# Optimization experiments

Measured on AMD Instinct MI355X. Metric: run time of the kernel, lower is better.

The kernel has to match this reference:

```python
import jax, jax.numpy as jnp
import numpy as np

VEC_DIM = 300
NUM_DOCS = 500000
NUM_WORDS = 100000
BATCH = 4096
NUM_CTX = 10
NUM_NOISE_P1 = 26


def setup_inputs() -> dict:
    key = jax.random.key(0)
    k1, k2, k3, k4, k5 = jax.random.split(key, 5)
    context_ids = jax.random.randint(k1, (BATCH, NUM_CTX), 0, NUM_WORDS)
    doc_ids = jax.random.randint(k2, (BATCH,), 0, NUM_DOCS)
    target_noise_ids = jax.random.randint(k3, (BATCH, NUM_NOISE_P1), 0, NUM_WORDS)
    D = jax.random.normal(k4, (NUM_DOCS, VEC_DIM), dtype=jnp.float32)
    W = jax.random.normal(k5, (NUM_WORDS, VEC_DIM), dtype=jnp.float32)
    O = jnp.zeros((VEC_DIM, NUM_WORDS), dtype=jnp.float32)
    return {
        "context_ids": context_ids,
        "doc_ids": doc_ids,
        "target_noise_ids": target_noise_ids,
        "D": D,
        "W": W,
        "O": O,
    }


def reference(context_ids, doc_ids, target_noise_ids, D, W, O):
    # x[b] = D[doc_ids[b]] + sum_c W[context_ids[b, c]]   -> (B, vec_dim)
    x = D[doc_ids] + jnp.sum(W[context_ids], axis=1)
    # O[:, target_noise_ids] gathered as O.T[target_noise_ids] -> (B, N, vec_dim)
    # scores[b, n] = x[b] . O[:, target_noise_ids[b, n]]
    scores = jnp.einsum("bd,bnd->bn", x, O.T[target_noise_ids])
    return scores
```

## Files before the change

kernel.cpp:

```cpp
#include <hip/hip_runtime.h>

#define VEC_DIM   300
#define VEC_F4    75
#define NUM_WORDS 100000
#define BATCH_N   4096
#define NUM_CTX   10
#define NUM_NOISE 26
#define TWORDS    32

__global__ __launch_bounds__(256) void transpose_kernel(
    const float* __restrict__ O,
    float*       __restrict__ OT)
{
    __shared__ float tile[TWORDS * VEC_DIM];
    const int wBase = blockIdx.x * TWORDS;
    const int tid   = threadIdx.x;

    for (int idx = tid; idx < VEC_DIM * (TWORDS / 4); idx += 256) {
        const int d = idx >> 3;
        const int c = idx & 7;
        const float4 v = *reinterpret_cast<const float4*>(
            O + (size_t)d * NUM_WORDS + wBase + 4 * c);
        tile[(4 * c + 0) * VEC_DIM + d] = v.x;
        tile[(4 * c + 1) * VEC_DIM + d] = v.y;
        tile[(4 * c + 2) * VEC_DIM + d] = v.z;
        tile[(4 * c + 3) * VEC_DIM + d] = v.w;
    }
    __syncthreads();

    for (int idx = tid; idx < TWORDS * VEC_F4; idx += 256) {
        const int w = idx / VEC_F4;
        const int c = idx - w * VEC_F4;
        const float4 v = *reinterpret_cast<const float4*>(tile + w * VEC_DIM + 4 * c);
        *reinterpret_cast<float4*>(OT + (size_t)(wBase + w) * VEC_DIM + 4 * c) = v;
    }
}

__global__ __launch_bounds__(256) void pvdm_score_kernel(
    const int*   __restrict__ context_ids,
    const int*   __restrict__ doc_ids,
    const int*   __restrict__ tn_ids,
    const float* __restrict__ D,
    const float* __restrict__ W,
    const float* __restrict__ OT,
    float*       __restrict__ out)
{
    __shared__ float4 xs4[VEC_F4];
    const int b   = blockIdx.x;
    const int tid = threadIdx.x;

    if (tid < VEC_F4) {
        const int doc = doc_ids[b];
        const float4* __restrict__ Drow =
            reinterpret_cast<const float4*>(D + (size_t)doc * VEC_DIM);
        float4 v = Drow[tid];
#pragma unroll
        for (int c = 0; c < NUM_CTX; ++c) {
            const int wd = context_ids[b * NUM_CTX + c];
            const float4 u =
                reinterpret_cast<const float4*>(W + (size_t)wd * VEC_DIM)[tid];
            v.x += u.x; v.y += u.y; v.z += u.z; v.w += u.w;
        }
        xs4[tid] = v;
    }
    __syncthreads();

    const int wave = tid >> 6;
    const int lane = tid & 63;

    const float4 xa = xs4[lane];
    float4 xb = make_float4(0.f, 0.f, 0.f, 0.f);
    if (lane < VEC_F4 - 64) xb = xs4[64 + lane];

    const int* __restrict__ tb = tn_ids + b * NUM_NOISE;

#pragma unroll
    for (int k = 0; k < 7; ++k) {
        const int n = wave + 4 * k;
        if (n < NUM_NOISE) {
            const int t = tb[n];
            const float4* __restrict__ row =
                reinterpret_cast<const float4*>(OT + (size_t)t * VEC_DIM);
            const float4 ra = row[lane];
            float s = ra.x * xa.x + ra.y * xa.y + ra.z * xa.z + ra.w * xa.w;
            if (lane < VEC_F4 - 64) {
                const float4 rb = row[64 + lane];
                s += rb.x * xb.x + rb.y * xb.y + rb.z * xb.z + rb.w * xb.w;
            }
#pragma unroll
            for (int off = 32; off > 0; off >>= 1)
                s += __shfl_down(s, off, 64);
            if (lane == 0) out[b * NUM_NOISE + n] = s;
        }
    }
}

__global__ __launch_bounds__(256) void pvdm_score_direct_kernel(
    const int*   __restrict__ context_ids,
    const int*   __restrict__ doc_ids,
    const int*   __restrict__ tn_ids,
    const float* __restrict__ D,
    const float* __restrict__ W,
    const float* __restrict__ O,
    float*       __restrict__ out)
{
    __shared__ float xs[VEC_DIM];
    const int b   = blockIdx.x;
    const int tid = threadIdx.x;
    const int doc = doc_ids[b];
    int ctx[NUM_CTX];
#pragma unroll
    for (int c = 0; c < NUM_CTX; ++c) ctx[c] = context_ids[b * NUM_CTX + c];
    for (int d = tid; d < VEC_DIM; d += 256) {
        float v = D[(size_t)doc * VEC_DIM + d];
#pragma unroll
        for (int c = 0; c < NUM_CTX; ++c)
            v += W[(size_t)ctx[c] * VEC_DIM + d];
        xs[d] = v;
    }
    __syncthreads();
    const int wave = tid >> 6;
    const int lane = tid & 63;
    for (int n = wave; n < NUM_NOISE; n += 4) {
        const int t = tn_ids[b * NUM_NOISE + n];
        float s = 0.0f;
        for (int d = lane; d < VEC_DIM; d += 64)
            s += xs[d] * O[(size_t)d * NUM_WORDS + t];
#pragma unroll
        for (int off = 32; off > 0; off >>= 1)
            s += __shfl_down(s, off, 64);
        if (lane == 0) out[b * NUM_NOISE + n] = s;
    }
}

extern "C" void kernel_launch(void* const* d_in, const int* in_sizes, int n_in,
                              void* d_out, int out_size, void* d_ws, size_t ws_size,
                              hipStream_t stream) {
    const int*   context_ids = (const int*)  d_in[0];
    const int*   doc_ids     = (const int*)  d_in[1];
    const int*   tn_ids      = (const int*)  d_in[2];
    const float* D           = (const float*)d_in[3];
    const float* W           = (const float*)d_in[4];
    const float* O           = (const float*)d_in[5];
    float*       out         = (float*)d_out;

    const size_t OT_BYTES = (size_t)NUM_WORDS * VEC_DIM * sizeof(float);

    if (ws_size >= OT_BYTES) {
        float* OT = (float*)d_ws;
        transpose_kernel<<<NUM_WORDS / TWORDS, 256, 0, stream>>>(O, OT);
        pvdm_score_kernel<<<BATCH_N, 256, 0, stream>>>(
            context_ids, doc_ids, tn_ids, D, W, OT, out);
    } else {
        pvdm_score_direct_kernel<<<BATCH_N, 256, 0, stream>>>(
            context_ids, doc_ids, tn_ids, D, W, O, out);
    }
}
```

Measured before the change: 809.2 us.

## Drop O transpose pass and gather strided columns of O directly

```diff
diff --git a/kernel.cpp b/kernel.cpp
--- a/kernel.cpp
+++ b/kernel.cpp
@@ -7,6 +7,72 @@
 #define NUM_CTX   10
 #define NUM_NOISE 26
 #define TWORDS    32
+
+
+__global__ __launch_bounds__(256) void pvdm_score_direct_kernel(
+    const int*   __restrict__ context_ids,
+    const int*   __restrict__ doc_ids,
+    const int*   __restrict__ tn_ids,
+    const float* __restrict__ D,
+    const float* __restrict__ W,
+    const float* __restrict__ O,
+    float*       __restrict__ out)
+{
+    __shared__ __align__(16) float xs[VEC_DIM];
+    const int b   = blockIdx.x;
+    const int tid = threadIdx.x;
+
+    if (tid < VEC_F4) {
+        const int doc = doc_ids[b];
+        float4 v = reinterpret_cast<const float4*>(D + (size_t)doc * VEC_DIM)[tid];
+#pragma unroll
+        for (int c = 0; c < NUM_CTX; ++c) {
+            const int wd = context_ids[b * NUM_CTX + c];
+            const float4 u =
+                reinterpret_cast<const float4*>(W + (size_t)wd * VEC_DIM)[tid];
+            v.x += u.x; v.y += u.y; v.z += u.z; v.w += u.w;
+        }
+        reinterpret_cast<float4*>(xs)[tid] = v;
+    }
+    __syncthreads();
+
+    const int wave = tid >> 6;
+    const int lane = tid & 63;
+
+    const float x0 = xs[lane];
+    const float x1 = xs[lane + 64];
+    const float x2 = xs[lane + 128];
+    const float x3 = xs[lane + 192];
+    const float x4 = (lane < VEC_DIM - 256) ? xs[lane + 256] : 0.0f;
+
+    const int* __restrict__ tb = tn_ids + b * NUM_NOISE;
+
+    int tv[7];
+#pragma unroll
+    for (int k = 0; k < 7; ++k) {
+        const int n = wave + 4 * k;
+        tv[k] = (n < NUM_NOISE) ? tb[n] : tb[0];
+    }
+
+#pragma unroll
+    for (int k = 0; k < 7; ++k) {
+        const int n = wave + 4 * k;
+        if (n < NUM_NOISE) {
+            const float* __restrict__ col = O + tv[k];
+            float s = x0 * col[(size_t)(lane      ) * NUM_WORDS]
+                    + x1 * col[(size_t)(lane +  64) * NUM_WORDS]
+                    + x2 * col[(size_t)(lane + 128) * NUM_WORDS]
+                    + x3 * col[(size_t)(lane + 192) * NUM_WORDS];
+            if (lane < VEC_DIM - 256)
+                s += x4 * col[(size_t)(lane + 256) * NUM_WORDS];
+#pragma unroll
+            for (int off = 32; off > 0; off >>= 1)
+                s += __shfl_down(s, off, 64);
+            if (lane == 0) out[b * NUM_NOISE + n] = s;
+        }
+    }
+}
+
 
 __global__ __launch_bounds__(256) void transpose_kernel(
     const float* __restrict__ O,
@@ -51,9 +117,7 @@
 
     if (tid < VEC_F4) {
         const int doc = doc_ids[b];
-        const float4* __restrict__ Drow =
-            reinterpret_cast<const float4*>(D + (size_t)doc * VEC_DIM);
-        float4 v = Drow[tid];
+        float4 v = reinterpret_cast<const float4*>(D + (size_t)doc * VEC_DIM)[tid];
 #pragma unroll
         for (int c = 0; c < NUM_CTX; ++c) {
             const int wd = context_ids[b * NUM_CTX + c];
@@ -95,44 +159,6 @@
     }
 }
 
-__global__ __launch_bounds__(256) void pvdm_score_direct_kernel(
-    const int*   __restrict__ context_ids,
-    const int*   __restrict__ doc_ids,
-    const int*   __restrict__ tn_ids,
-    const float* __restrict__ D,
-    const float* __restrict__ W,
-    const float* __restrict__ O,
-    float*       __restrict__ out)
-{
-    __shared__ float xs[VEC_DIM];
-    const int b   = blockIdx.x;
-    const int tid = threadIdx.x;
-    const int doc = doc_ids[b];
-    int ctx[NUM_CTX];
-#pragma unroll
-    for (int c = 0; c < NUM_CTX; ++c) ctx[c] = context_ids[b * NUM_CTX + c];
-    for (int d = tid; d < VEC_DIM; d += 256) {
-        float v = D[(size_t)doc * VEC_DIM + d];
-#pragma unroll
-        for (int c = 0; c < NUM_CTX; ++c)
-            v += W[(size_t)ctx[c] * VEC_DIM + d];
-        xs[d] = v;
-    }
-    __syncthreads();
-    const int wave = tid >> 6;
-    const int lane = tid & 63;
-    for (int n = wave; n < NUM_NOISE; n += 4) {
-        const int t = tn_ids[b * NUM_NOISE + n];
-        float s = 0.0f;
-        for (int d = lane; d < VEC_DIM; d += 64)
-            s += xs[d] * O[(size_t)d * NUM_WORDS + t];
-#pragma unroll
-        for (int off = 32; off > 0; off >>= 1)
-            s += __shfl_down(s, off, 64);
-        if (lane == 0) out[b * NUM_NOISE + n] = s;
-    }
-}
-
 extern "C" void kernel_launch(void* const* d_in, const int* in_sizes, int n_in,
                               void* d_out, int out_size, void* d_ws, size_t ws_size,
                               hipStream_t stream) {
@@ -144,15 +170,7 @@
     const float* O           = (const float*)d_in[5];
     float*       out         = (float*)d_out;
 
-    const size_t OT_BYTES = (size_t)NUM_WORDS * VEC_DIM * sizeof(float);
-
-    if (ws_size >= OT_BYTES) {
-        float* OT = (float*)d_ws;
-        transpose_kernel<<<NUM_WORDS / TWORDS, 256, 0, stream>>>(O, OT);
-        pvdm_score_kernel<<<BATCH_N, 256, 0, stream>>>(
-            context_ids, doc_ids, tn_ids, D, W, OT, out);
-    } else {
-        pvdm_score_direct_kernel<<<BATCH_N, 256, 0, stream>>>(
-            context_ids, doc_ids, tn_ids, D, W, O, out);
-    }
+    (void)d_ws; (void)ws_size;
+    pvdm_score_direct_kernel<<<BATCH_N, 256, 0, stream>>>(
+        context_ids, doc_ids, tn_ids, D, W, O, out);
 }
```

After: 1.289 ms. 1.59x slower.

## Bucket noise targets by word chunk and score against one streamed pass of O

Applied to the files above, without the earlier changes.

```diff
diff --git a/kernel.cpp b/kernel.cpp
--- a/kernel.cpp
+++ b/kernel.cpp
@@ -2,20 +2,124 @@
 
 #define VEC_DIM   300
 #define VEC_F4    75
+#define NUM_DOCS  500000
 #define NUM_WORDS 100000
 #define BATCH_N   4096
 #define NUM_CTX   10
 #define NUM_NOISE 26
-#define TWORDS    32
+
+#define WB        32
+#define NCHUNK    (NUM_WORDS / WB)
+#define CAP       192
+
+#define WS_X_OFF        0
+#define WS_CNT_OFF      (8u << 20)
+#define WS_BKT_OFF      ((8u << 20) + (64u << 10))
+#define WS_NEEDED       (WS_BKT_OFF + (size_t)NCHUNK * CAP * 4)
+
+__global__ __launch_bounds__(256) void zero_counters_kernel(int* __restrict__ cnt)
+{
+    const int i = blockIdx.x * 256 + threadIdx.x;
+    if (i < NCHUNK) cnt[i] = 0;
+}
+
+__global__ __launch_bounds__(128) void build_scatter_kernel(
+    const int*   __restrict__ context_ids,
+    const int*   __restrict__ doc_ids,
+    const int*   __restrict__ tn_ids,
+    const float* __restrict__ D,
+    const float* __restrict__ W,
+    float*       __restrict__ X,
+    int*         __restrict__ counters,
+    unsigned*    __restrict__ buckets)
+{
+    const int b   = blockIdx.x;
+    const int tid = threadIdx.x;
+
+    if (tid < VEC_F4) {
+        const int doc = doc_ids[b];
+        float4 v = reinterpret_cast<const float4*>(D + (size_t)doc * VEC_DIM)[tid];
+#pragma unroll
+        for (int c = 0; c < NUM_CTX; ++c) {
+            const int wd = context_ids[b * NUM_CTX + c];
+            const float4 u =
+                reinterpret_cast<const float4*>(W + (size_t)wd * VEC_DIM)[tid];
+            v.x += u.x; v.y += u.y; v.z += u.z; v.w += u.w;
+        }
+        reinterpret_cast<float4*>(X + (size_t)b * VEC_DIM)[tid] = v;
+    } else if (tid < VEC_F4 + NUM_NOISE) {
+        const int n = tid - VEC_F4;
+        const int t = tn_ids[b * NUM_NOISE + n];
+        const int chunk = t >> 5;
+        const int tc    = t & (WB - 1);
+        const int pos   = atomicAdd(&counters[chunk], 1);
+        if (pos < CAP)
+            buckets[(size_t)chunk * CAP + pos] =
+                ((unsigned)b << 10) | ((unsigned)n << 5) | (unsigned)tc;
+    }
+}
+
+__global__ __launch_bounds__(256) void chunk_score_kernel(
+    const float*    __restrict__ O,
+    const float*    __restrict__ X,
+    const int*      __restrict__ counters,
+    const unsigned* __restrict__ buckets,
+    float*          __restrict__ out)
+{
+    __shared__ float tile[WB][VEC_DIM];
+    const int chunk = blockIdx.x;
+    const int tid   = threadIdx.x;
+    const int w0    = chunk * WB;
+
+    int cnt = counters[chunk];
+    if (cnt > CAP) cnt = CAP;
+
+#pragma unroll
+    for (int k = 0; k < 10; ++k) {
+        const int d  = (tid >> 3) + (k << 5);
+        const int jj = tid & 7;
+        if (d < VEC_DIM) {
+            const float4 v = *reinterpret_cast<const float4*>(
+                O + (size_t)d * NUM_WORDS + w0 + 4 * jj);
+            tile[4 * jj + 0][d] = v.x;
+            tile[4 * jj + 1][d] = v.y;
+            tile[4 * jj + 2][d] = v.z;
+            tile[4 * jj + 3][d] = v.w;
+        }
+    }
+    __syncthreads();
+
+    const int wave = tid >> 6;
+    const int lane = tid & 63;
+
+    for (int p = wave; p < cnt; p += 4) {
+        const unsigned e = buckets[(size_t)chunk * CAP + p];
+        const int tc = e & 31;
+        const int n  = (e >> 5) & 31;
+        const int b  = e >> 10;
+        const float* __restrict__ xr = X + (size_t)b * VEC_DIM;
+
+        float s = tile[tc][lane]       * xr[lane]
+                + tile[tc][lane +  64] * xr[lane +  64]
+                + tile[tc][lane + 128] * xr[lane + 128]
+                + tile[tc][lane + 192] * xr[lane + 192];
+        if (lane < VEC_DIM - 256)
+            s += tile[tc][lane + 256] * xr[lane + 256];
+#pragma unroll
+        for (int off = 32; off > 0; off >>= 1)
+            s += __shfl_down(s, off, 64);
+        if (lane == 0) out[b * NUM_NOISE + n] = s;
+    }
+}
+
+#define TWORDS 32
 
 __global__ __launch_bounds__(256) void transpose_kernel(
-    const float* __restrict__ O,
-    float*       __restrict__ OT)
+    const float* __restrict__ O, float* __restrict__ OT)
 {
     __shared__ float tile[TWORDS * VEC_DIM];
     const int wBase = blockIdx.x * TWORDS;
     const int tid   = threadIdx.x;
-
     for (int idx = tid; idx < VEC_DIM * (TWORDS / 4); idx += 256) {
         const int d = idx >> 3;
         const int c = idx & 7;
@@ -27,7 +131,6 @@
         tile[(4 * c + 3) * VEC_DIM + d] = v.w;
     }
     __syncthreads();
-
     for (int idx = tid; idx < TWORDS * VEC_F4; idx += 256) {
         const int w = idx / VEC_F4;
         const int c = idx - w * VEC_F4;
@@ -37,23 +140,17 @@
 }
 
 __global__ __launch_bounds__(256) void pvdm_score_kernel(
-    const int*   __restrict__ context_ids,
-    const int*   __restrict__ doc_ids,
-    const int*   __restrict__ tn_ids,
-    const float* __restrict__ D,
-    const float* __restrict__ W,
-    const float* __restrict__ OT,
-    float*       __restrict__ out)
+    const int* __restrict__ context_ids, const int* __restrict__ doc_ids,
+    const int* __restrict__ tn_ids, const float* __restrict__ D,
+    const float* __restrict__ W, const float* __restrict__ OT,
+    float* __restrict__ out)
 {
     __shared__ float4 xs4[VEC_F4];
     const int b   = blockIdx.x;
     const int tid = threadIdx.x;
-
     if (tid < VEC_F4) {
         const int doc = doc_ids[b];
-        const float4* __restrict__ Drow =
-            reinterpret_cast<const float4*>(D + (size_t)doc * VEC_DIM);
-        float4 v = Drow[tid];
+        float4 v = reinterpret_cast<const float4*>(D + (size_t)doc * VEC_DIM)[tid];
 #pragma unroll
         for (int c = 0; c < NUM_CTX; ++c) {
             const int wd = context_ids[b * NUM_CTX + c];
@@ -64,16 +161,12 @@
         xs4[tid] = v;
     }
     __syncthreads();
-
     const int wave = tid >> 6;
     const int lane = tid & 63;
-
     const float4 xa = xs4[lane];
     float4 xb = make_float4(0.f, 0.f, 0.f, 0.f);
     if (lane < VEC_F4 - 64) xb = xs4[64 + lane];
-
     const int* __restrict__ tb = tn_ids + b * NUM_NOISE;
-
 #pragma unroll
     for (int k = 0; k < 7; ++k) {
         const int n = wave + 4 * k;
@@ -96,13 +189,10 @@
 }
 
 __global__ __launch_bounds__(256) void pvdm_score_direct_kernel(
-    const int*   __restrict__ context_ids,
-    const int*   __restrict__ doc_ids,
-    const int*   __restrict__ tn_ids,
-    const float* __restrict__ D,
-    const float* __restrict__ W,
-    const float* __restrict__ O,
-    float*       __restrict__ out)
+    const int* __restrict__ context_ids, const int* __restrict__ doc_ids,
+    const int* __restrict__ tn_ids, const float* __restrict__ D,
+    const float* __restrict__ W, const float* __restrict__ O,
+    float* __restrict__ out)
 {
     __shared__ float xs[VEC_DIM];
     const int b   = blockIdx.x;
@@ -144,9 +234,18 @@
     const float* O           = (const float*)d_in[5];
     float*       out         = (float*)d_out;
 
-    const size_t OT_BYTES = (size_t)NUM_WORDS * VEC_DIM * sizeof(float);
-
-    if (ws_size >= OT_BYTES) {
+    if (ws_size >= WS_NEEDED) {
+        char* ws = (char*)d_ws;
+        float*    X        = (float*)   (ws + WS_X_OFF);
+        int*      counters = (int*)     (ws + WS_CNT_OFF);
+        unsigned* buckets  = (unsigned*)(ws + WS_BKT_OFF);
+
+        zero_counters_kernel<<<(NCHUNK + 255) / 256, 256, 0, stream>>>(counters);
+        build_scatter_kernel<<<BATCH_N, 128, 0, stream>>>(
+            context_ids, doc_ids, tn_ids, D, W, X, counters, buckets);
+        chunk_score_kernel<<<NCHUNK, 256, 0, stream>>>(
+            O, X, counters, buckets, out);
+    } else if (ws_size >= (size_t)NUM_WORDS * VEC_DIM * sizeof(float)) {
         float* OT = (float*)d_ws;
         transpose_kernel<<<NUM_WORDS / TWORDS, 256, 0, stream>>>(O, OT);
         pvdm_score_kernel<<<BATCH_N, 256, 0, stream>>>(
```

Result: no change. 804.6 us (-0.6%).
